# Kernel tuning notes

Hardware: AMD Instinct MI355X
Metric: run time of the kernel (lower is better)

The kernel has to match this reference:

```python
import jax, jax.numpy as jnp
import numpy as np

E = 64      # encoding_size (hard-coded in MatchingNetwork)
K = 5       # processing_steps


def _cell(x, h, c, Wih, Whh, bih, bhh):
    # PyTorch LSTMCell: gates ordered i, f, g, o
    z = x @ Wih.T + h @ Whh.T + bih + bhh
    i, f, g, o = jnp.split(z, 4, axis=-1)
    c2 = jax.nn.sigmoid(f) * c + jax.nn.sigmoid(i) * jnp.tanh(g)
    h2 = jax.nn.sigmoid(o) * jnp.tanh(c2)
    return h2, c2


def _lstm_seq(xs, Wih, Whh, bih, bhh, reverse=False):
    # xs: [B, S, E] -> per-step hidden states [B, S, E]
    B = xs.shape[0]
    xs_t = jnp.swapaxes(xs, 0, 1)  # [S, B, E]
    if reverse:
        xs_t = xs_t[::-1]
    h0 = jnp.zeros((B, Wih.shape[0] // 4), xs.dtype)

    def step(carry, x_t):
        h, c = carry
        h2, c2 = _cell(x_t, h, c, Wih, Whh, bih, bhh)
        return (h2, c2), h2

    _, hs = jax.lax.scan(step, (h0, h0), xs_t)
    if reverse:
        hs = hs[::-1]
    return jnp.swapaxes(hs, 0, 1)


def setup_inputs() -> dict:
    key = jax.random.key(0)
    ks = jax.random.split(key, 16)
    B, N, k, T, L, V = 64, 20, 10, 128, 40, 32000
    support_tokens = jax.random.randint(ks[0], (B, N, k, L), 0, V)
    target_tokens = jax.random.randint(ks[1], (B, T, L), 0, V)
    emb = jax.random.normal(ks[2], (V, E), jnp.float32) * 0.1
    emb = emb.at[0].set(0.0)  # padding_idx row
    s = 1.0 / np.sqrt(E)

    def lstm_params(k1, k2, k3, k4):
        return (jax.random.uniform(k1, (4 * E, E), jnp.float32, -s, s),
                jax.random.uniform(k2, (4 * E, E), jnp.float32, -s, s),
                jax.random.uniform(k3, (4 * E,), jnp.float32, -s, s),
                jax.random.uniform(k4, (4 * E,), jnp.float32, -s, s))

    f_Wih, f_Whh, f_bih, f_bhh = lstm_params(ks[3], ks[4], ks[5], ks[6])
    gf_Wih, gf_Whh, gf_bih, gf_bhh = lstm_params(ks[7], ks[8], ks[9], ks[10])
    gb_Wih, gb_Whh, gb_bih, gb_bhh = lstm_params(ks[11], ks[12], ks[13], ks[14])
    return {
        'support_tokens': support_tokens, 'target_tokens': target_tokens,
        'emb': emb,
        'f_Wih': f_Wih, 'f_Whh': f_Whh, 'f_bih': f_bih, 'f_bhh': f_bhh,
        'gf_Wih': gf_Wih, 'gf_Whh': gf_Whh, 'gf_bih': gf_bih, 'gf_bhh': gf_bhh,
        'gb_Wih': gb_Wih, 'gb_Whh': gb_Whh, 'gb_bih': gb_bih, 'gb_bhh': gb_bhh,
    }


def reference(support_tokens, target_tokens, emb,
              f_Wih, f_Whh, f_bih, f_bhh,
              gf_Wih, gf_Whh, gf_bih, gf_bhh,
              gb_Wih, gb_Whh, gb_bih, gb_bhh):
    B, N, kk, L = support_tokens.shape
    T = target_tokens.shape[1]

    # EncodingLayer: embedding lookup + sum-pool over sentence length
    sup_enc = emb[support_tokens].sum(axis=3)   # [B, N, k, E]
    tgt_enc = emb[target_tokens].sum(axis=2)    # [B, T, E]

    # GLayer: bidirectional LSTM over flattened support, sum dirs + residual
    flat = sup_enc.reshape(B, N * kk, E)
    hf = _lstm_seq(flat, gf_Wih, gf_Whh, gf_bih, gf_bhh, reverse=False)
    hb = _lstm_seq(flat, gb_Wih, gb_Whh, gb_bih, gb_bhh, reverse=True)
    sup_emb = (hf + hb).reshape(B, N, kk, E) + sup_enc  # [B, N, k, E]

    # FLayer: K-step attention LSTM over targets
    x = tgt_enc.reshape(B * T, E)
    h = jnp.zeros_like(x)
    c = jnp.zeros_like(x)
    r = jnp.zeros_like(x)
    for _ in range(K):
        h = h + r
        h_next, c = _cell(x, h, c, f_Wih, f_Whh, f_bih, f_bhh)
        h_next = h_next + x
        scores = jnp.einsum('bte,bnke->btnk', h.reshape(B, T, E), sup_emb)
        att = jax.nn.softmax(scores.reshape(B, T, N * kk), axis=2).reshape(B, T, N, kk)
        r = jnp.einsum('btnk,bnke->bte', att, sup_emb).reshape(B * T, E)
        h = h_next
    tgt_emb = h.reshape(B, T, E)

    # Cosine-similarity attention over support set (softmax over N*k)
    num = jnp.einsum('bte,bnke->btnk', tgt_emb, sup_emb)
    tn = jnp.linalg.norm(tgt_emb, axis=-1)          # [B, T]
    sn = jnp.linalg.norm(sup_emb, axis=-1)          # [B, N, k]
    sims = num / jnp.maximum(tn[:, :, None, None] * sn[:, None, :, :], 1e-8)
    attention = jax.nn.softmax(sims.reshape(B, T, N * kk), axis=2).reshape(B, T, N, kk)
    return attention
```

## Files before the change

### kernel.cpp

```cpp
#include <hip/hip_runtime.h>

#define Bn   64
#define Tn   128
#define NKn  200
#define En   64
#define Ln   40

__device__ __forceinline__ float sigm_f(float x){ return 1.0f/(1.0f+__expf(-x)); }
__device__ __forceinline__ float tanh_f(float x){ float e=__expf(2.0f*x); return 1.0f-2.0f/(e+1.0f); }
__device__ __forceinline__ float rdl(float v, int ln){
  return __uint_as_float(__builtin_amdgcn_readlane(__float_as_uint(v), (unsigned)ln));
}

__global__ __launch_bounds__(256) void embed_all(const int* __restrict__ sup,
                                                 const int* __restrict__ tgt,
                                                 const float* __restrict__ emb,
                                                 float* __restrict__ sup_enc,
                                                 float* __restrict__ tgt_enc){
  int tid = threadIdx.x;
  int gr  = blockIdx.x*16 + (tid>>4);
  int e4  = tid & 15;
  const int* tr; float* out;
  if (gr < 12800){ tr = sup + (size_t)gr*Ln;        out = sup_enc + (size_t)gr*64; }
  else           { int r2=gr-12800; tr = tgt + (size_t)r2*Ln; out = tgt_enc + (size_t)r2*64; }
  float4 acc = {0.f,0.f,0.f,0.f};
  #pragma unroll 4
  for (int t=0;t<Ln;t++){
    int tok = tr[t];
    float4 v = ((const float4*)emb)[(size_t)tok*16 + e4];
    acc.x+=v.x; acc.y+=v.y; acc.z+=v.z; acc.w+=v.w;
  }
  ((float4*)out)[e4] = acc;
}

__global__ __launch_bounds__(256,1) void gemm_sup2(const float* __restrict__ x,
                                                   const float* __restrict__ Wa, const float* __restrict__ Wb,
                                                   const float* __restrict__ ba1,const float* __restrict__ ba2,
                                                   const float* __restrict__ bb1,const float* __restrict__ bb2,
                                                   float* __restrict__ outa, float* __restrict__ outb){
  int tid=threadIdx.x, l=tid&63, w=tid>>6;
  int g=tid;
  int m0 = blockIdx.x*16;
  __shared__ __attribute__((aligned(16))) float xs[16*64];
  #pragma unroll
  for(int q=0;q<4;q++){ int r=4*w+q; xs[r*64+l]=x[(size_t)(m0+r)*64+l]; }
  float wa[64], wb[64];
  {
    const float4* A4=(const float4*)(Wa + (size_t)g*64);
    const float4* B4=(const float4*)(Wb + (size_t)g*64);
    #pragma unroll
    for(int q=0;q<16;q++){
      float4 va=A4[q]; wa[4*q]=va.x; wa[4*q+1]=va.y; wa[4*q+2]=va.z; wa[4*q+3]=va.w;
      float4 vb=B4[q]; wb[4*q]=vb.x; wb[4*q+1]=vb.y; wb[4*q+2]=vb.z; wb[4*q+3]=vb.w;
    }
  }
  float biasa=ba1[g]+ba2[g], biasb=bb1[g]+bb2[g];
  __syncthreads();
  #pragma unroll
  for(int r=0;r<16;r++){
    const float4* x4=(const float4*)&xs[r*64];
    float a0=biasa,a1=0.f,b0=biasb,b1=0.f;
    #pragma unroll
    for(int kc=0;kc<16;kc++){
      float4 h4=x4[kc];
      a0=fmaf(wa[4*kc+0],h4.x,a0); b0=fmaf(wb[4*kc+0],h4.x,b0);
      a1=fmaf(wa[4*kc+1],h4.y,a1); b1=fmaf(wb[4*kc+1],h4.y,b1);
      a0=fmaf(wa[4*kc+2],h4.z,a0); b0=fmaf(wb[4*kc+2],h4.z,b0);
      a1=fmaf(wa[4*kc+3],h4.w,a1); b1=fmaf(wb[4*kc+3],h4.w,b1);
    }
    outa[(size_t)(m0+r)*256+g]=a0+a1;
    outb[(size_t)(m0+r)*256+g]=b0+b1;
  }
}

__global__ __launch_bounds__(256,1) void lstm_seq(const float* __restrict__ xg_f,
                                                  const float* __restrict__ xg_b,
                                                  const float* __restrict__ Whh_f,
                                                  const float* __restrict__ Whh_b,
                                                  float* __restrict__ hf,
                                                  float* __restrict__ hb){
  int tid=threadIdx.x, l=tid&63, w=tid>>6;
  int dir=blockIdx.x>>6, b=blockIdx.x&63;
  const float* xg = dir? xg_b : xg_f;
  const float* Whh= dir? Whh_b: Whh_f;
  float* out = dir? hb : hf;
  float wr[64];
  const float4* W4=(const float4*)(Whh+(size_t)(w*64+l)*64);
  #pragma unroll
  for(int q=0;q<16;q++){ float4 v=W4[q]; wr[4*q]=v.x; wr[4*q+1]=v.y; wr[4*q+2]=v.z; wr[4*q+3]=v.w; }
  __shared__ float z_s[2][256];
  float h=0.f, c=0.f;
  const int tstart = dir?(NKn-1):0, dt = dir?-1:1;
  const float* xgb = xg + (size_t)b*NKn*256 + w*64 + l;
  float xv = xgb[(size_t)tstart*256];
  for(int s=0;s<NKn;s++){
    int t=tstart+s*dt;
    float xnx=0.f;
    if (s<NKn-1) xnx = xgb[(size_t)(t+dt)*256];
    float a0=xv,a1=0.f,a2=0.f,a3=0.f;
    #pragma unroll
    for(int q=0;q<16;q++){
      a0=fmaf(wr[4*q+0],rdl(h,4*q+0),a0);
      a1=fmaf(wr[4*q+1],rdl(h,4*q+1),a1);
      a2=fmaf(wr[4*q+2],rdl(h,4*q+2),a2);
      a3=fmaf(wr[4*q+3],rdl(h,4*q+3),a3);
    }
    z_s[s&1][tid]=(a0+a1)+(a2+a3);
    __syncthreads();
    float zi=z_s[s&1][l], zf=z_s[s&1][64+l], zg=z_s[s&1][128+l], zo=z_s[s&1][192+l];
    c = sigm_f(zf)*c + sigm_f(zi)*tanh_f(zg);
    h = sigm_f(zo)*tanh_f(c);
    if(w==0) out[((size_t)b*NKn+t)*64+l]=h;
    xv=xnx;
  }
}

__global__ __launch_bounds__(256,2) void gemmz_combine(const float* __restrict__ tgt_enc,
                                                       const float* __restrict__ W,
                                                       const float* __restrict__ b1,
                                                       const float* __restrict__ b2,
                                                       float* __restrict__ zx,
                                                       const float* __restrict__ hf,
                                                       const float* __restrict__ hb,
                                                       const float* __restrict__ sup_enc,
                                                       float* __restrict__ semb,
                                                       float* __restrict__ sn){
  int tid=threadIdx.x, l=tid&63, w=tid>>6;
  int blk=blockIdx.x;
  if (blk < 512){
    int g=tid, m0=blk*16;
    __shared__ __attribute__((aligned(16))) float xs[16*64];
    #pragma unroll
    for(int q=0;q<4;q++){ int r=4*w+q; xs[r*64+l]=tgt_enc[(size_t)(m0+r)*64+l]; }
    float wr[64];
    const float4* W4=(const float4*)(W + (size_t)g*64);
    #pragma unroll
    for(int q=0;q<16;q++){ float4 v=W4[q]; wr[4*q]=v.x; wr[4*q+1]=v.y; wr[4*q+2]=v.z; wr[4*q+3]=v.w; }
    float bias=b1[g]+b2[g];
    __syncthreads();
    #pragma unroll
    for(int r=0;r<16;r++){
      const float4* x4=(const float4*)&xs[r*64];
      float a0=bias,a1=0.f,a2=0.f,a3=0.f;
      #pragma unroll
      for(int kc=0;kc<16;kc++){
        float4 h4=x4[kc];
        a0=fmaf(wr[4*kc+0],h4.x,a0);
        a1=fmaf(wr[4*kc+1],h4.y,a1);
        a2=fmaf(wr[4*kc+2],h4.z,a2);
        a3=fmaf(wr[4*kc+3],h4.w,a3);
      }
      zx[(size_t)(m0+r)*256+g]=(a0+a1)+(a2+a3);
    }
  } else {
    int m0=(blk-512)*16;
    #pragma unroll
    for(int q=0;q<4;q++){
      size_t m=(size_t)m0 + w*4 + q;
      float v = hf[m*64+l] + hb[m*64+l] + sup_enc[m*64+l];
      semb[m*64+l]=v;
      float s=v*v;
      #pragma unroll
      for (int o=32;o>0;o>>=1) s += __shfl_xor(s,o,64);
      if (l==0) sn[m]=sqrtf(s);
    }
  }
}

__global__ __launch_bounds__(256,1) void fused_K(const float* __restrict__ zx,
                                                 const float* __restrict__ Whh,
                                                 const float* __restrict__ x,
                                                 const float* __restrict__ semb,
                                                 const float* __restrict__ sn,
                                                 float* __restrict__ out){
  int tid=threadIdx.x, l=tid&63, w=tid>>6;
  int b=blockIdx.x>>3, t0=(blockIdx.x&7)*16;
  int m0=b*Tn+t0;
  int g=tid;
  bool valid = g<NKn;
  const float* sbase = semb + (size_t)b*NKn*64;
  __shared__ __attribute__((aligned(16))) float hu_s[16*64];
  __shared__ __attribute__((aligned(16))) float sbuf[16*256];
  __shared__ __attribute__((aligned(16))) float hn_s[16*64];
  __shared__ float wredA[64], wredB[64];
  float wr[64], s4f[64];
  {
    const float4* W4=(const float4*)(Whh+(size_t)g*64);
    #pragma unroll
    for(int q=0;q<16;q++){ float4 v=W4[q]; wr[4*q]=v.x; wr[4*q+1]=v.y; wr[4*q+2]=v.z; wr[4*q+3]=v.w; }
  }
  if(valid){
    const float4* sp=(const float4*)(sbase+(size_t)g*64);
    #pragma unroll
    for(int q=0;q<16;q++){ float4 v=sp[q]; s4f[4*q]=v.x; s4f[4*q+1]=v.y; s4f[4*q+2]=v.z; s4f[4*q+3]=v.w; }
  } else {
    #pragma unroll
    for(int q=0;q<64;q++) s4f[q]=0.f;
  }
  float zxr[16];
  #pragma unroll
  for(int r=0;r<16;r++) zxr[r]=zx[(size_t)(m0+r)*256+g];
  float xr[4];
  #pragma unroll
  for(int q=0;q<4;q++) xr[q]=x[(size_t)(m0+q*4+w)*64+l];
  float snr = valid ? sn[(size_t)b*NKn+g] : 1.f;
  float cq[4]={0.f,0.f,0.f,0.f};
  float scr[16], ex[16], mx[16];
  for(int k=0;k<5;k++){
    if(k==0){
      #pragma unroll
      for(int r=0;r<16;r++){ sbuf[r*256+g]=zxr[r]; scr[r]=0.f; }
    } else {
      #pragma unroll
      for(int r=0;r<16;r++){
        float z0=zxr[r], z1=0.f, sc0=0.f, sc1=0.f;
        const float4* h4p=(const float4*)&hu_s[r*64];
        #pragma unroll
        for(int kc=0;kc<16;kc++){
          float4 h4=h4p[kc];
          z0 =fmaf(wr[4*kc+0] ,h4.x,z0 ); sc0=fmaf(s4f[4*kc+0],h4.x,sc0);
          z1 =fmaf(wr[4*kc+1] ,h4.y,z1 ); sc1=fmaf(s4f[4*kc+1],h4.y,sc1);
          z0 =fmaf(wr[4*kc+2] ,h4.z,z0 ); sc0=fmaf(s4f[4*kc+2],h4.z,sc0);
          z1 =fmaf(wr[4*kc+3] ,h4.w,z1 ); sc1=fmaf(s4f[4*kc+3],h4.w,sc1);
        }
        sbuf[r*256+g]=z0+z1;
        scr[r]=sc0+sc1;
      }
    }
    __syncthreads();
    #pragma unroll
    for(int q=0;q<4;q++){
      int r=q*4+w;
      float zi=sbuf[r*256+l], zf=sbuf[r*256+64+l], zg=sbuf[r*256+128+l], zo=sbuf[r*256+192+l];
      float c=sigm_f(zf)*cq[q]+sigm_f(zi)*tanh_f(zg);
      cq[q]=c;
      hn_s[r*64+l]=sigm_f(zo)*tanh_f(c)+xr[q];
    }
    if(k<4){
      #pragma unroll
      for(int t=0;t<16;t++){
        float m = valid ? scr[t] : -1e30f;
        #pragma unroll
        for(int o=32;o>0;o>>=1) m=fmaxf(m,__shfl_xor(m,o,64));
        mx[t]=m;
      }
      if(l==0){
        #pragma unroll
        for(int t=0;t<16;t++) wredA[t*4+w]=mx[t];
      }
      __syncthreads();
      #pragma unroll
      for(int t=0;t<16;t++){
        const float4 m4=*(const float4*)&wredA[t*4];
        float gm=fmaxf(fmaxf(m4.x,m4.y),fmaxf(m4.z,m4.w));
        float e=valid?__expf(scr[t]-gm):0.f;
        ex[t]=e;
        float s=e;
        #pragma unroll
        for(int o=32;o>0;o>>=1) s+=__shfl_xor(s,o,64);
        mx[t]=s;
      }
      if(l==0){
        #pragma unroll
        for(int t=0;t<16;t++) wredB[t*4+w]=mx[t];
      }
      __syncthreads();
      #pragma unroll
      for(int t=0;t<16;t++){
        const float4 s4v=*(const float4*)&wredB[t*4];
        float tot=(s4v.x+s4v.y)+(s4v.z+s4v.w);
        ex[t]*=1.0f/tot;
      }
      if(valid){
        #pragma unroll
        for(int cg=0;cg<4;cg++)
          *(float4*)&sbuf[g*20+4*cg]=make_float4(ex[4*cg+0],ex[4*cg+1],ex[4*cg+2],ex[4*cg+3]);
      }
      __syncthreads();
      float r0=0.f,r1=0.f,r2=0.f,r3=0.f;
      #pragma unroll 8
      for(int j=0;j<NKn;j++){
        float4 a4=*(const float4*)&sbuf[j*20+w*4];
        float sv=sbase[(size_t)j*64+l];
        r0=fmaf(a4.x,sv,r0);
        r1=fmaf(a4.y,sv,r1);
        r2=fmaf(a4.z,sv,r2);
        r3=fmaf(a4.w,sv,r3);
      }
      int rb=w*4;
      hu_s[(rb+0)*64+l]=r0 + hn_s[(rb+0)*64+l];
      hu_s[(rb+1)*64+l]=r1 + hn_s[(rb+1)*64+l];
      hu_s[(rb+2)*64+l]=r2 + hn_s[(rb+2)*64+l];
      hu_s[(rb+3)*64+l]=r3 + hn_s[(rb+3)*64+l];
      __syncthreads();
    }
  }
  __syncthreads();
  float tnorm[16];
  #pragma unroll
  for(int t=0;t<16;t++){
    float v=hn_s[t*64+l];
    float s=v*v;
    #pragma unroll
    for(int o=32;o>0;o>>=1) s+=__shfl_xor(s,o,64);
    tnorm[t]=sqrtf(s);
  }
  #pragma unroll
  for(int t=0;t<16;t++){
    const float4* h4p=(const float4*)&hn_s[t*64];
    float a0=0.f,a1=0.f;
    #pragma unroll
    for(int kc=0;kc<16;kc++){
      float4 h4=h4p[kc];
      a0=fmaf(s4f[4*kc+0],h4.x,a0);
      a1=fmaf(s4f[4*kc+1],h4.y,a1);
      a0=fmaf(s4f[4*kc+2],h4.z,a0);
      a1=fmaf(s4f[4*kc+3],h4.w,a1);
    }
    scr[t]=(a0+a1) / fmaxf(tnorm[t]*snr,1e-8f);
  }
  #pragma unroll
  for(int t=0;t<16;t++){
    float m = valid ? scr[t] : -1e30f;
    #pragma unroll
    for(int o=32;o>0;o>>=1) m=fmaxf(m,__shfl_xor(m,o,64));
    mx[t]=m;
  }
  if(l==0){
    #pragma unroll
    for(int t=0;t<16;t++) wredA[t*4+w]=mx[t];
  }
  __syncthreads();
  #pragma unroll
  for(int t=0;t<16;t++){
    const float4 m4=*(const float4*)&wredA[t*4];
    float gm=fmaxf(fmaxf(m4.x,m4.y),fmaxf(m4.z,m4.w));
    float e=valid?__expf(scr[t]-gm):0.f;
    ex[t]=e;
    float s=e;
    #pragma unroll
    for(int o=32;o>0;o>>=1) s+=__shfl_xor(s,o,64);
    mx[t]=s;
  }
  if(l==0){
    #pragma unroll
    for(int t=0;t<16;t++) wredB[t*4+w]=mx[t];
  }
  __syncthreads();
  #pragma unroll
  for(int t=0;t<16;t++){
    const float4 s4v=*(const float4*)&wredB[t*4];
    float tot=(s4v.x+s4v.y)+(s4v.z+s4v.w);
    if(valid) out[((size_t)(m0+t))*NKn + g]=ex[t]*(1.0f/tot);
  }
}

extern "C" void kernel_launch(void* const* d_in, const int* in_sizes, int n_in,
                              void* d_out, int out_size, void* d_ws, size_t ws_size,
                              hipStream_t stream) {
  (void)in_sizes; (void)n_in; (void)out_size; (void)ws_size;
  const int*   sup_toks = (const int*)d_in[0];
  const int*   tgt_toks = (const int*)d_in[1];
  const float* emb      = (const float*)d_in[2];
  const float* f_Wih    = (const float*)d_in[3];
  const float* f_Whh    = (const float*)d_in[4];
  const float* f_bih    = (const float*)d_in[5];
  const float* f_bhh    = (const float*)d_in[6];
  const float* gf_Wih   = (const float*)d_in[7];
  const float* gf_Whh   = (const float*)d_in[8];
  const float* gf_bih   = (const float*)d_in[9];
  const float* gf_bhh   = (const float*)d_in[10];
  const float* gb_Wih   = (const float*)d_in[11];
  const float* gb_Whh   = (const float*)d_in[12];
  const float* gb_bih   = (const float*)d_in[13];
  const float* gb_bhh   = (const float*)d_in[14];

  float* ws = (float*)d_ws;
  float* sup_enc = ws;
  float* tgt_enc = sup_enc + 819200;
  float* bufA    = tgt_enc + 524288;
  float* bufB    = bufA    + 3276800;
  float* semb    = bufB    + 3276800;
  float* hb      = semb    + 819200;
  float* sn      = hb      + 819200;

  float* xg_f = bufA;
  float* xg_b = bufB;

  embed_all<<<1312,256,0,stream>>>(sup_toks, tgt_toks, emb, sup_enc, tgt_enc);
  gemm_sup2<<<800,256,0,stream>>>(sup_enc, gf_Wih, gb_Wih,
                                  gf_bih, gf_bhh, gb_bih, gb_bhh, xg_f, xg_b);
  lstm_seq<<<128,256,0,stream>>>(xg_f, xg_b, gf_Whh, gb_Whh, semb , hb);

  float* zx = bufA;

  gemmz_combine<<<1312,256,0,stream>>>(tgt_enc, f_Wih, f_bih, f_bhh, zx,
                                       semb, hb, sup_enc, semb, sn);

  fused_K<<<512,256,0,stream>>>(zx, f_Whh, tgt_enc, semb, sn, (float*)d_out);
}
```

Before: 351.2 us.

## Overlap target-gate GEMM with the sequential support LSTM in one launch

The f-LSTM input GEMM over target encodings moves into spare blocks of the recurrent support-LSTM kernel. Its 128 latency-bound blocks leave most CUs idle, so those CUs now compute zx into a dedicated workspace buffer, and the combine/norm step becomes its own small kernel. The support-set input GEMM also doubles rows per block (32 instead of 16) to reuse the register-held weights more. This needs extra workspace, and the old path is kept as a fallback when the workspace is too small.

```diff
diff --git a/kernel.cpp b/kernel.cpp
--- a/kernel.cpp
+++ b/kernel.cpp
@@ -40,10 +40,10 @@
                                                    float* __restrict__ outa, float* __restrict__ outb){
   int tid=threadIdx.x, l=tid&63, w=tid>>6;
   int g=tid;
-  int m0 = blockIdx.x*16;
-  __shared__ __attribute__((aligned(16))) float xs[16*64];
-  #pragma unroll
-  for(int q=0;q<4;q++){ int r=4*w+q; xs[r*64+l]=x[(size_t)(m0+r)*64+l]; }
+  int m0 = blockIdx.x*32;
+  __shared__ __attribute__((aligned(16))) float xs[32*64];
+  #pragma unroll
+  for(int q=0;q<8;q++){ int r=8*w+q; xs[r*64+l]=x[(size_t)(m0+r)*64+l]; }
   float wa[64], wb[64];
   {
     const float4* A4=(const float4*)(Wa + (size_t)g*64);
@@ -57,7 +57,7 @@
   float biasa=ba1[g]+ba2[g], biasb=bb1[g]+bb2[g];
   __syncthreads();
   #pragma unroll
-  for(int r=0;r<16;r++){
+  for(int r=0;r<32;r++){
     const float4* x4=(const float4*)&xs[r*64];
     float a0=biasa,a1=0.f,b0=biasb,b1=0.f;
     #pragma unroll
@@ -73,45 +73,78 @@
   }
 }
 
-__global__ __launch_bounds__(256,1) void lstm_seq(const float* __restrict__ xg_f,
-                                                  const float* __restrict__ xg_b,
-                                                  const float* __restrict__ Whh_f,
-                                                  const float* __restrict__ Whh_b,
-                                                  float* __restrict__ hf,
-                                                  float* __restrict__ hb){
+__global__ __launch_bounds__(256,1) void lstm_zx(const float* __restrict__ xg_f,
+                                                 const float* __restrict__ xg_b,
+                                                 const float* __restrict__ Whh_f,
+                                                 const float* __restrict__ Whh_b,
+                                                 float* __restrict__ hf,
+                                                 float* __restrict__ hb,
+                                                 const float* __restrict__ tgt_enc,
+                                                 const float* __restrict__ Wih,
+                                                 const float* __restrict__ bih,
+                                                 const float* __restrict__ bhh,
+                                                 float* __restrict__ zx){
   int tid=threadIdx.x, l=tid&63, w=tid>>6;
-  int dir=blockIdx.x>>6, b=blockIdx.x&63;
-  const float* xg = dir? xg_b : xg_f;
-  const float* Whh= dir? Whh_b: Whh_f;
-  float* out = dir? hb : hf;
-  float wr[64];
-  const float4* W4=(const float4*)(Whh+(size_t)(w*64+l)*64);
-  #pragma unroll
-  for(int q=0;q<16;q++){ float4 v=W4[q]; wr[4*q]=v.x; wr[4*q+1]=v.y; wr[4*q+2]=v.z; wr[4*q+3]=v.w; }
-  __shared__ float z_s[2][256];
-  float h=0.f, c=0.f;
-  const int tstart = dir?(NKn-1):0, dt = dir?-1:1;
-  const float* xgb = xg + (size_t)b*NKn*256 + w*64 + l;
-  float xv = xgb[(size_t)tstart*256];
-  for(int s=0;s<NKn;s++){
-    int t=tstart+s*dt;
-    float xnx=0.f;
-    if (s<NKn-1) xnx = xgb[(size_t)(t+dt)*256];
-    float a0=xv,a1=0.f,a2=0.f,a3=0.f;
-    #pragma unroll
-    for(int q=0;q<16;q++){
-      a0=fmaf(wr[4*q+0],rdl(h,4*q+0),a0);
-      a1=fmaf(wr[4*q+1],rdl(h,4*q+1),a1);
-      a2=fmaf(wr[4*q+2],rdl(h,4*q+2),a2);
-      a3=fmaf(wr[4*q+3],rdl(h,4*q+3),a3);
-    }
-    z_s[s&1][tid]=(a0+a1)+(a2+a3);
+  int blk=blockIdx.x;
+  if (blk < 128){
+    int dir=blk>>6, b=blk&63;
+    const float* xg = dir? xg_b : xg_f;
+    const float* Whh= dir? Whh_b: Whh_f;
+    float* out = dir? hb : hf;
+    float wr[64];
+    const float4* W4=(const float4*)(Whh+(size_t)(w*64+l)*64);
+    #pragma unroll
+    for(int q=0;q<16;q++){ float4 v=W4[q]; wr[4*q]=v.x; wr[4*q+1]=v.y; wr[4*q+2]=v.z; wr[4*q+3]=v.w; }
+    __shared__ float z_s[2][256];
+    float h=0.f, c=0.f;
+    const int tstart = dir?(NKn-1):0, dt = dir?-1:1;
+    const float* xgb = xg + (size_t)b*NKn*256 + w*64 + l;
+    float xv = xgb[(size_t)tstart*256];
+    for(int s=0;s<NKn;s++){
+      int t=tstart+s*dt;
+      float xnx=0.f;
+      if (s<NKn-1) xnx = xgb[(size_t)(t+dt)*256];
+      float a0=xv,a1=0.f,a2=0.f,a3=0.f;
+      #pragma unroll
+      for(int q=0;q<16;q++){
+        a0=fmaf(wr[4*q+0],rdl(h,4*q+0),a0);
+        a1=fmaf(wr[4*q+1],rdl(h,4*q+1),a1);
+        a2=fmaf(wr[4*q+2],rdl(h,4*q+2),a2);
+        a3=fmaf(wr[4*q+3],rdl(h,4*q+3),a3);
+      }
+      z_s[s&1][tid]=(a0+a1)+(a2+a3);
+      __syncthreads();
+      float zi=z_s[s&1][l], zf=z_s[s&1][64+l], zg=z_s[s&1][128+l], zo=z_s[s&1][192+l];
+      c = sigm_f(zf)*c + sigm_f(zi)*tanh_f(zg);
+      h = sigm_f(zo)*tanh_f(c);
+      if(w==0) out[((size_t)b*NKn+t)*64+l]=h;
+      xv=xnx;
+    }
+  } else {
+    int g=tid, m0=(blk-128)*16;
+    __shared__ __attribute__((aligned(16))) float xs[16*64];
+    #pragma unroll
+    for(int q=0;q<4;q++){ int r=4*w+q; xs[r*64+l]=tgt_enc[(size_t)(m0+r)*64+l]; }
+    float wr[64];
+    const float4* W4=(const float4*)(Wih + (size_t)g*64);
+    #pragma unroll
+    for(int q=0;q<16;q++){ float4 v=W4[q]; wr[4*q]=v.x; wr[4*q+1]=v.y; wr[4*q+2]=v.z; wr[4*q+3]=v.w; }
+    float bias=bih[g]+bhh[g];
     __syncthreads();
-    float zi=z_s[s&1][l], zf=z_s[s&1][64+l], zg=z_s[s&1][128+l], zo=z_s[s&1][192+l];
-    c = sigm_f(zf)*c + sigm_f(zi)*tanh_f(zg);
-    h = sigm_f(zo)*tanh_f(c);
-    if(w==0) out[((size_t)b*NKn+t)*64+l]=h;
-    xv=xnx;
+    #pragma unroll
+    for(int r=0;r<16;r++){
+      const float4* x4=(const float4*)&xs[r*64];
+      float a0=bias,a1=0.f,a2=0.f,a3=0.f;
+      #pragma unroll
+      for(int kc=0;kc<16;kc++){
+        float4 h4=x4[kc];
+        a0=fmaf(wr[4*kc+0],h4.x,a0);
+        a1=fmaf(wr[4*kc+1],h4.y,a1);
+        a2=fmaf(wr[4*kc+2],h4.z,a2);
+        a3=fmaf(wr[4*kc+3],h4.w,a3);
+      }
+      zx[(size_t)(m0+r)*256+g]=(a0+a1)+(a2+a3);
+    }
   }
 }
 
@@ -164,6 +197,25 @@
       for (int o=32;o>0;o>>=1) s += __shfl_xor(s,o,64);
       if (l==0) sn[m]=sqrtf(s);
     }
+  }
+}
+
+__global__ __launch_bounds__(256,2) void combine(const float* __restrict__ hf,
+                                                 const float* __restrict__ hb,
+                                                 const float* __restrict__ sup_enc,
+                                                 float* __restrict__ semb,
+                                                 float* __restrict__ sn){
+  int tid=threadIdx.x, l=tid&63, w=tid>>6;
+  int m0=blockIdx.x*16;
+  #pragma unroll
+  for(int q=0;q<4;q++){
+    size_t m=(size_t)m0 + w*4 + q;
+    float v = hf[m*64+l] + hb[m*64+l] + sup_enc[m*64+l];
+    semb[m*64+l]=v;
+    float s=v*v;
+    #pragma unroll
+    for (int o=32;o>0;o>>=1) s += __shfl_xor(s,o,64);
+    if (l==0) sn[m]=sqrtf(s);
   }
 }
 
@@ -358,7 +410,7 @@
 extern "C" void kernel_launch(void* const* d_in, const int* in_sizes, int n_in,
                               void* d_out, int out_size, void* d_ws, size_t ws_size,
                               hipStream_t stream) {
-  (void)in_sizes; (void)n_in; (void)out_size; (void)ws_size;
+  (void)in_sizes; (void)n_in; (void)out_size;
   const int*   sup_toks = (const int*)d_in[0];
   const int*   tgt_toks = (const int*)d_in[1];
   const float* emb      = (const float*)d_in[2];
@@ -383,19 +435,28 @@
   float* semb    = bufB    + 3276800;
   float* hb      = semb    + 819200;
   float* sn      = hb      + 819200;
+  float* zx_ded  = sn      + 12800;
 
   float* xg_f = bufA;
   float* xg_b = bufB;
 
+  const size_t need_mega = (size_t)(819200+524288+3276800+3276800+819200+819200+12800+2097152)*sizeof(float);
+
   embed_all<<<1312,256,0,stream>>>(sup_toks, tgt_toks, emb, sup_enc, tgt_enc);
-  gemm_sup2<<<800,256,0,stream>>>(sup_enc, gf_Wih, gb_Wih,
+  gemm_sup2<<<400,256,0,stream>>>(sup_enc, gf_Wih, gb_Wih,
                                   gf_bih, gf_bhh, gb_bih, gb_bhh, xg_f, xg_b);
-  lstm_seq<<<128,256,0,stream>>>(xg_f, xg_b, gf_Whh, gb_Whh, semb , hb);
-
-  float* zx = bufA;
-
-  gemmz_combine<<<1312,256,0,stream>>>(tgt_enc, f_Wih, f_bih, f_bhh, zx,
-                                       semb, hb, sup_enc, semb, sn);
-
-  fused_K<<<512,256,0,stream>>>(zx, f_Whh, tgt_enc, semb, sn, (float*)d_out);
-}
+
+  if (ws_size >= need_mega){
+    lstm_zx<<<640,256,0,stream>>>(xg_f, xg_b, gf_Whh, gb_Whh, semb , hb,
+                                  tgt_enc, f_Wih, f_bih, f_bhh, zx_ded);
+    combine<<<800,256,0,stream>>>(semb, hb, sup_enc, semb, sn);
+    fused_K<<<512,256,0,stream>>>(zx_ded, f_Whh, tgt_enc, semb, sn, (float*)d_out);
+  } else {
+    lstm_zx<<<128,256,0,stream>>>(xg_f, xg_b, gf_Whh, gb_Whh, semb , hb,
+                                  tgt_enc, f_Wih, f_bih, f_bhh, (float*)d_ws );
+    float* zx = bufA;
+    gemmz_combine<<<1312,256,0,stream>>>(tgt_enc, f_Wih, f_bih, f_bhh, zx,
+                                         semb, hb, sup_enc, semb, sn);
+    fused_K<<<512,256,0,stream>>>(zx, f_Whh, tgt_enc, semb, sn, (float*)d_out);
+  }
+}
```

Result: no change. 354.4 us (+0.9%).
